# Performance work log

Hardware: AMD Instinct MI355X
Metric: run time of the kernel (lower is better)

The kernel has to match this reference:

```python
import jax, jax.numpy as jnp
import numpy as np

DIM = 512
NH = 16
HEAD = DIM // NH  # 32
WS1 = 8   # window_size // 2 (shift_h=True)
WS2 = 16  # window_size
SHIFT = 4  # window_size // 4


def _rotary(t, cos, sin):
    # t: (..., C); split even/odd channels, rotate, concat halves
    x1, x2 = t[..., 0::2], t[..., 1::2]
    return jnp.concatenate([x1 * cos - x2 * sin, x2 * cos + x1 * sin], axis=-1)


def setup_inputs() -> dict:
    key = jax.random.key(0)
    ks = jax.random.split(key, 8)
    B, H, W = 8, 64, 64
    G = (H // WS1) * (W // WS2)  # 32
    N = WS1 * WS2                # 128
    s = 1.0 / np.sqrt(DIM)
    return {
        "x": jax.random.normal(ks[0], (B, H, W, DIM), jnp.float32),
        "pos_embed_q": jax.random.normal(ks[1], (2, G, 1, N, HEAD // 2), jnp.float32),
        "pos_embed_kv": jax.random.normal(ks[2], (2, G, 1, 2 * N, HEAD // 2), jnp.float32),
        "mask": jnp.zeros((G, 1, N, 2 * N), jnp.float32),
        "w_q": jax.random.normal(ks[3], (DIM, DIM), jnp.float32) * s,
        "b_q": jnp.zeros((DIM,), jnp.float32),
        "w_kv": jax.random.normal(ks[4], (DIM, 2 * DIM), jnp.float32) * s,
        "b_kv": jnp.zeros((2 * DIM,), jnp.float32),
        "w_proj": jax.random.normal(ks[5], (DIM, DIM), jnp.float32) * s,
        "b_proj": jnp.zeros((DIM,), jnp.float32),
        "H": H,
        "W": W,
    }


def reference(x, pos_embed_q, pos_embed_kv, mask, w_q, b_q, w_kv, b_kv, w_proj, b_proj, H, W):
    B = x.shape[0]
    G = (H // WS1) * (W // WS2)
    N = WS1 * WS2
    C = HEAD

    # q projection + window partition -> (B, G, nH, N, C)
    q = x @ w_q + b_q
    q = q.reshape(B, H // WS1, WS1, W // WS2, WS2, NH, C)
    q = q.transpose(0, 1, 3, 5, 2, 4, 6).reshape(B, G, NH, N, C)

    # kv projection, two opposite rolls along H, window partition -> (2, B, G, nH, 2N, C)
    kv = x @ w_kv + b_kv                              # (B,H,W,2D)
    kvs = jnp.stack([jnp.roll(kv, -SHIFT, axis=1), jnp.roll(kv, SHIFT, axis=1)])  # (2shift,B,H,W,2D)
    kvs = kvs.reshape(2, B, H // WS1, WS1, W // WS2, WS2, 2, NH, C)
    kvs = kvs.transpose(6, 1, 2, 4, 7, 0, 3, 5, 8).reshape(2, B, G, NH, 2 * N, C)
    k, v = kvs[0], kvs[1]

    # rotary position embedding
    q = _rotary(q, pos_embed_q[0], pos_embed_q[1])
    k = _rotary(k, pos_embed_kv[0], pos_embed_kv[1])

    # scaled dot product attention with additive mask (eval: no dropout)
    scale = 1.0 / np.sqrt(C)
    scores = jnp.einsum('bgnqc,bgnkc->bgnqk', q, k) * scale + mask
    attn = jax.nn.softmax(scores, axis=-1)
    o = jnp.einsum('bgnqk,bgnkc->bgnqc', attn, v)     # (B,G,nH,N,C)

    # window un-partition -> (B, H, W, D), output projection
    o = o.reshape(B, H // WS1, W // WS2, NH, WS1, WS2, C)
    o = o.transpose(0, 1, 4, 2, 5, 3, 6).reshape(B, H, W, DIM)
    return o @ w_proj + b_proj
```

## Files before the change

### kernel.cpp

```cpp
#include <hip/hip_runtime.h>

typedef __bf16 bf16x8 __attribute__((ext_vector_type(8)));
typedef __bf16 bf16x4 __attribute__((ext_vector_type(4)));
typedef float f32x4 __attribute__((ext_vector_type(4)));

#define DEV __device__ __forceinline__

DEV f32x4 mfma16(bf16x8 a, bf16x8 b, f32x4 c) {
    return __builtin_amdgcn_mfma_f32_16x16x32_bf16(a, b, c, 0, 0, 0);
}

DEV void async16(const void* g, void* l) {
    __builtin_amdgcn_global_load_lds((__attribute__((address_space(1))) void*)g,
                                     (__attribute__((address_space(3))) void*)l, 16, 0, 0);
}

#define LDS_FENCE() asm volatile("" ::: "memory")

__global__ __launch_bounds__(256) void cast_x_kernel(const float4* __restrict__ in,
                                                     bf16x8* __restrict__ out) {
    int i = blockIdx.x * 256 + threadIdx.x;
    float4 a = in[2 * i], b = in[2 * i + 1];
    bf16x8 o;
    o[0] = (__bf16)a.x; o[1] = (__bf16)a.y; o[2] = (__bf16)a.z; o[3] = (__bf16)a.w;
    o[4] = (__bf16)b.x; o[5] = (__bf16)b.y; o[6] = (__bf16)b.z; o[7] = (__bf16)b.w;
    out[i] = o;
}

__global__ void transpose_cast_kernel(const float* __restrict__ src,
                                      __bf16* __restrict__ dst, int R, int C) {
    __shared__ float tile[32][33];
    int tx = threadIdx.x, ty = threadIdx.y;
    int c0 = blockIdx.x * 32, r0 = blockIdx.y * 32;
#pragma unroll
    for (int j = 0; j < 4; ++j)
        tile[ty + j * 8][tx] = src[(size_t)(r0 + ty + j * 8) * C + c0 + tx];
    __syncthreads();
#pragma unroll
    for (int j = 0; j < 4; ++j)
        dst[(size_t)(c0 + ty + j * 8) * R + r0 + tx] = (__bf16)tile[tx][ty + j * 8];
}

__global__ __launch_bounds__(256) void mask_flag_kernel(const float* __restrict__ mask,
                                                        int* __restrict__ flags) {
    int g = blockIdx.x;
    const float4* m4 = (const float4*)(mask + (size_t)g * 32768);
    int any = 0;
    for (int i = threadIdx.x; i < 8192; i += 256) {
        float4 v = m4[i];
        any |= (v.x != 0.f) | (v.y != 0.f) | (v.z != 0.f) | (v.w != 0.f);
    }
    any = __any(any) ? 1 : 0;
    __shared__ int s;
    if (threadIdx.x == 0) s = 0;
    __syncthreads();
    if ((threadIdx.x & 63) == 0 && any) atomicOr(&s, 1);
    __syncthreads();
    if (threadIdx.x == 0) flags[g] = s;
}

__global__ __launch_bounds__(256) void gemm_bt(const __bf16* __restrict__ A,
                                               const __bf16* __restrict__ Bt,
                                               const float* __restrict__ bias0,
                                               const float* __restrict__ bias1,
                                               void* __restrict__ Cout, int N, int mode) {
    __shared__ __bf16 As[128 * 64];
    __shared__ __bf16 Bs[128 * 64];
    const int tid = threadIdx.x;
    const int bm = blockIdx.x, bn = blockIdx.y;
    const int lane = tid & 63, wv = tid >> 6;
    const int quad = lane >> 4, l16 = lane & 15;
    const int wm = (wv & 1) * 64, wn = (wv >> 1) * 64;
    const __bf16* Abase = A + (size_t)bm * 128 * 512;
    const __bf16* Bbase = Bt + (size_t)bn * 128 * 512;
    f32x4 acc[4][4] = {};
    for (int kr = 0; kr < 8; ++kr) {
#pragma unroll
        for (int i = 0; i < 4; ++i) {
            int chunk = i * 256 + tid;
            int r = chunk >> 3, cc = chunk & 7;
            int src = cc ^ (r & 7);
            async16(Abase + r * 512 + kr * 64 + src * 8, &As[chunk * 8]);
            async16(Bbase + r * 512 + kr * 64 + src * 8, &Bs[chunk * 8]);
        }
        __syncthreads();
#pragma unroll
        for (int kk = 0; kk < 2; ++kk) {
            bf16x8 af[4], bfm[4];
#pragma unroll
            for (int t = 0; t < 4; ++t) {
                int ra = wm + t * 16 + l16, rb = wn + t * 16 + l16;
                int c = kk * 4 + quad;
                af[t]  = *(const bf16x8*)&As[ra * 64 + ((c ^ (ra & 7)) << 3)];
                bfm[t] = *(const bf16x8*)&Bs[rb * 64 + ((c ^ (rb & 7)) << 3)];
            }
#pragma unroll
            for (int mt = 0; mt < 4; ++mt)
#pragma unroll
                for (int nt = 0; nt < 4; ++nt)
                    acc[mt][nt] = mfma16(af[mt], bfm[nt], acc[mt][nt]);
        }
        __syncthreads();
    }
#pragma unroll
    for (int nt = 0; nt < 4; ++nt) {
        int ng = bn * 128 + wn + nt * 16 + l16;
        float bias = (ng < 512) ? bias0[ng] : bias1[ng - 512];
        if (mode == 0) {
            int type = ng >> 9, nhh = (ng >> 5) & 15, c = ng & 31;
            __bf16* dst = (__bf16*)Cout + (size_t)type * 16777216 + (size_t)nhh * 1048576 + c;
#pragma unroll
            for (int mt = 0; mt < 4; ++mt)
#pragma unroll
                for (int r = 0; r < 4; ++r) {
                    int mg = bm * 128 + wm + mt * 16 + quad * 4 + r;
                    dst[(size_t)mg * 32] = (__bf16)(acc[mt][nt][r] + bias);
                }
        } else {
#pragma unroll
            for (int mt = 0; mt < 4; ++mt)
#pragma unroll
                for (int r = 0; r < 4; ++r) {
                    int mg = bm * 128 + wm + mt * 16 + quad * 4 + r;
                    ((float*)Cout)[(size_t)mg * N + ng] = acc[mt][nt][r] + bias;
                }
        }
    }
}

#define ATT_SCALE 0.17677669529663687f

__global__ __launch_bounds__(256, 4) void attn_kernel(const __bf16* __restrict__ qkv,
                                                      const float* __restrict__ peq,
                                                      const float* __restrict__ pekv,
                                                      const float* __restrict__ mask,
                                                      const int* __restrict__ mflags,
                                                      __bf16* __restrict__ oatt) {
    __shared__ __align__(16) char smem[38400];
    __bf16* Ks = (__bf16*)smem;
    __bf16* Vt = (__bf16*)(smem + 16384);
    __bf16* Ps = (__bf16*)(smem + 33280);

    const int tid = threadIdx.x;
    const int bid = ((blockIdx.x & 7) << 9) | (blockIdx.x >> 3);
    const int b = bid >> 9;
    const int g = (bid >> 4) & 31;
    const int nh = bid & 15;
    const int gh = g >> 2, gw = g & 3;
    const int lane = tid & 63, wv = tid >> 6;
    const int quad = lane >> 4, l16 = lane & 15;

    const __bf16* qq = qkv + (size_t)nh * 1048576;
    const __bf16* kkp = qkv + 16777216 + (size_t)nh * 1048576;
    const __bf16* vvp = qkv + 33554432 + (size_t)nh * 1048576;

#pragma unroll
    for (int it = 0; it < 4; ++it) {
        int item = it * 256 + tid;
        int ko = item >> 2, c8 = item & 3;
        int roll = ko >> 7, n = ko & 127;
        int h = (gh * 8 + (n >> 4) + (roll ? 60 : 4)) & 63;
        int w = gw * 16 + (n & 15);
        int row = (b * 64 + h) * 64 + w;
        bf16x8 v = *(const bf16x8*)(kkp + (size_t)row * 32 + c8 * 8);
        int pidx = (g * 256 + ko) * 16 + c8 * 4;
        float4 c4 = *(const float4*)(pekv + pidx);
        float4 s4 = *(const float4*)(pekv + 131072 + pidx);
        float cs[4] = {c4.x, c4.y, c4.z, c4.w}, sn[4] = {s4.x, s4.y, s4.z, s4.w};
        bf16x4 lo, hi;
#pragma unroll
        for (int j = 0; j < 4; ++j) {
            float k0 = (float)v[2 * j], k1 = (float)v[2 * j + 1];
            lo[j] = (__bf16)(k0 * cs[j] - k1 * sn[j]);
            hi[j] = (__bf16)(k1 * cs[j] + k0 * sn[j]);
        }
        int sw = (ko >> 1) & 3;
        int base = ko * 32, off = (c8 & 1) * 4;
        *(bf16x4*)&Ks[base + (((c8 >> 1) ^ sw) << 3) + off]       = lo;
        *(bf16x4*)&Ks[base + (((2 + (c8 >> 1)) ^ sw) << 3) + off] = hi;
    }
#pragma unroll
    for (int it = 0; it < 4; ++it) {
        int ko = tid;
        int roll = ko >> 7, n = ko & 127;
        int h = (gh * 8 + (n >> 4) + (roll ? 60 : 4)) & 63;
        int w = gw * 16 + (n & 15);
        int row = (b * 64 + h) * 64 + w;
        bf16x8 v = *(const bf16x8*)(vvp + (size_t)row * 32 + it * 8);
#pragma unroll
        for (int j = 0; j < 8; ++j)
            Vt[(it * 8 + j) * 264 + ko] = v[j];
    }

    bf16x8 aq[2];
    {
        const int halfsel = quad & 1;
        const bool hi_half = quad >= 2;
#pragma unroll
        for (int rt = 0; rt < 2; ++rt) {
            int n = wv * 32 + rt * 16 + l16;
            int h = gh * 8 + (n >> 4), w = gw * 16 + (n & 15);
            int row = (b * 64 + h) * 64 + w;
            const __bf16* qp = qq + (size_t)row * 32 + halfsel * 16;
            bf16x8 rA = *(const bf16x8*)qp;
            bf16x8 rB = *(const bf16x8*)(qp + 8);
            int pb = (g * 128 + n) * 16 + halfsel * 8;
            float4 ca = *(const float4*)(peq + pb);
            float4 cb = *(const float4*)(peq + pb + 4);
            float4 sa = *(const float4*)(peq + 65536 + pb);
            float4 sb = *(const float4*)(peq + 65536 + pb + 4);
            float cc[8] = {ca.x, ca.y, ca.z, ca.w, cb.x, cb.y, cb.z, cb.w};
            float ss[8] = {sa.x, sa.y, sa.z, sa.w, sb.x, sb.y, sb.z, sb.w};
#pragma unroll
            for (int j = 0; j < 8; ++j) {
                float q0 = (float)(j < 4 ? rA[2 * j] : rB[2 * (j - 4)]);
                float q1 = (float)(j < 4 ? rA[2 * j + 1] : rB[2 * (j - 4) + 1]);
                float r = hi_half ? (q1 * cc[j] + q0 * ss[j]) : (q0 * cc[j] - q1 * ss[j]);
                aq[rt][j] = (__bf16)(r * ATT_SCALE);
            }
        }
    }
    __syncthreads();

    f32x4 o00 = {}, o01 = {}, o10 = {}, o11 = {};
    f32x4 rs0 = {}, rs1 = {};
    const bool use_mask = mflags[g] != 0;
    const float* mg = mask + (size_t)g * 32768;
    __bf16* Pw = Ps + wv * 640;
    const int arow = l16 * 40 + quad * 8;

#pragma unroll 2
    for (int ch = 0; ch < 8; ++ch) {
        bf16x8 vb0 = *(const bf16x8*)&Vt[l16 * 264 + ch * 32 + quad * 8];
        bf16x8 vb1 = *(const bf16x8*)&Vt[(16 + l16) * 264 + ch * 32 + quad * 8];
        f32x4 z = {0.f, 0.f, 0.f, 0.f};
        int key0 = ch * 32 + l16, key1 = key0 + 16;
        bf16x8 bk0 = *(const bf16x8*)&Ks[key0 * 32 + ((quad ^ ((key0 >> 1) & 3)) << 3)];
        bf16x8 bk1 = *(const bf16x8*)&Ks[key1 * 32 + ((quad ^ ((key1 >> 1) & 3)) << 3)];
        f32x4 s00 = mfma16(aq[0], bk0, z), s01 = mfma16(aq[0], bk1, z);
        f32x4 s10 = mfma16(aq[1], bk0, z), s11 = mfma16(aq[1], bk1, z);

        if (use_mask) {
#pragma unroll
            for (int r = 0; r < 4; ++r) {
                int r0 = (wv * 32 + quad * 4 + r) * 256 + ch * 32 + l16;
                int r1 = (wv * 32 + 16 + quad * 4 + r) * 256 + ch * 32 + l16;
                s00[r] += mg[r0];      s01[r] += mg[r0 + 16];
                s10[r] += mg[r1];      s11[r] += mg[r1 + 16];
            }
        }
#pragma unroll
        for (int r = 0; r < 4; ++r) {
            s00[r] = __expf(s00[r]); s01[r] = __expf(s01[r]);
            s10[r] = __expf(s10[r]); s11[r] = __expf(s11[r]);
            rs0[r] += s00[r] + s01[r];
            rs1[r] += s10[r] + s11[r];
        }
#pragma unroll
        for (int r = 0; r < 4; ++r) {
            Pw[(quad * 4 + r) * 40 + l16]      = (__bf16)s00[r];
            Pw[(quad * 4 + r) * 40 + 16 + l16] = (__bf16)s01[r];
        }
        LDS_FENCE();
        bf16x8 a0 = *(const bf16x8*)&Pw[arow];
        LDS_FENCE();
#pragma unroll
        for (int r = 0; r < 4; ++r) {
            Pw[(quad * 4 + r) * 40 + l16]      = (__bf16)s10[r];
            Pw[(quad * 4 + r) * 40 + 16 + l16] = (__bf16)s11[r];
        }
        LDS_FENCE();
        bf16x8 a1 = *(const bf16x8*)&Pw[arow];
        LDS_FENCE();
        o00 = mfma16(a0, vb0, o00); o01 = mfma16(a0, vb1, o01);
        o10 = mfma16(a1, vb0, o10); o11 = mfma16(a1, vb1, o11);
    }

#pragma unroll
    for (int off = 1; off < 16; off <<= 1) {
#pragma unroll
        for (int r = 0; r < 4; ++r) {
            rs0[r] += __shfl_xor(rs0[r], off);
            rs1[r] += __shfl_xor(rs1[r], off);
        }
    }
#pragma unroll
    for (int r = 0; r < 4; ++r) { rs0[r] = 1.f / rs0[r]; rs1[r] = 1.f / rs1[r]; }

#pragma unroll
    for (int r = 0; r < 4; ++r) {
        {
            int rown = wv * 32 + quad * 4 + r;
            int h = gh * 8 + (rown >> 4), w = gw * 16 + (rown & 15);
            size_t base = ((size_t)(b * 64 + h) * 64 + w) * 512 + nh * 32;
            oatt[base + l16]      = (__bf16)(o00[r] * rs0[r]);
            oatt[base + 16 + l16] = (__bf16)(o01[r] * rs0[r]);
        }
        {
            int rown = wv * 32 + 16 + quad * 4 + r;
            int h = gh * 8 + (rown >> 4), w = gw * 16 + (rown & 15);
            size_t base = ((size_t)(b * 64 + h) * 64 + w) * 512 + nh * 32;
            oatt[base + l16]      = (__bf16)(o10[r] * rs1[r]);
            oatt[base + 16 + l16] = (__bf16)(o11[r] * rs1[r]);
        }
    }
}

extern "C" void kernel_launch(void* const* d_in, const int* in_sizes, int n_in,
                              void* d_out, int out_size, void* d_ws, size_t ws_size,
                              hipStream_t stream) {
    const float* x     = (const float*)d_in[0];
    const float* peq   = (const float*)d_in[1];
    const float* pekv  = (const float*)d_in[2];
    const float* mask  = (const float*)d_in[3];
    const float* wq    = (const float*)d_in[4];
    const float* bq    = (const float*)d_in[5];
    const float* wkv   = (const float*)d_in[6];
    const float* bkv   = (const float*)d_in[7];
    const float* wproj = (const float*)d_in[8];
    const float* bproj = (const float*)d_in[9];
    float* out = (float*)d_out;

    char* ws = (char*)d_ws;
    __bf16* xb    = (__bf16*)(ws);
    __bf16* oatt  = (__bf16*)(ws);
    __bf16* wqkvT = (__bf16*)(ws + 33554432);
    int*    mflag = (int*)(ws + 33554432);
    __bf16* wpT   = (__bf16*)(ws + 35127296);
    __bf16* qkv   = (__bf16*)(ws + 35651584);

    cast_x_kernel<<<8192, 256, 0, stream>>>((const float4*)x, (bf16x8*)xb);
    transpose_cast_kernel<<<dim3(16, 16), dim3(32, 8), 0, stream>>>(wq, wqkvT, 512, 512);
    transpose_cast_kernel<<<dim3(32, 16), dim3(32, 8), 0, stream>>>(wkv, wqkvT + 512 * 512, 512, 1024);
    transpose_cast_kernel<<<dim3(16, 16), dim3(32, 8), 0, stream>>>(wproj, wpT, 512, 512);

    gemm_bt<<<dim3(256, 12), 256, 0, stream>>>(xb, wqkvT, bq, bkv, qkv, 1536, 0);
    mask_flag_kernel<<<32, 256, 0, stream>>>(mask, mflag);
    attn_kernel<<<4096, 256, 0, stream>>>(qkv, peq, pekv, mask, mflag, oatt);
    gemm_bt<<<dim3(256, 4), 256, 0, stream>>>(oatt, wpT, bproj, bproj, out, 512, 1);
}
```

Measured before the change: 327.0 us.

## Replace GEMM with 256x256 tiled, double-buffered LDS pipeline and 512 threads

```diff
diff --git a/kernel.cpp b/kernel.cpp
--- a/kernel.cpp
+++ b/kernel.cpp
@@ -16,6 +16,8 @@
 }
 
 #define LDS_FENCE() asm volatile("" ::: "memory")
+#define BARRIER() asm volatile("s_barrier" ::: "memory")
+#define VMCNT(n) asm volatile("s_waitcnt vmcnt(" #n ")" ::: "memory")
 
 __global__ __launch_bounds__(256) void cast_x_kernel(const float4* __restrict__ in,
                                                      bf16x8* __restrict__ out) {
@@ -59,69 +61,100 @@
     if (threadIdx.x == 0) flags[g] = s;
 }
 
-__global__ __launch_bounds__(256) void gemm_bt(const __bf16* __restrict__ A,
-                                               const __bf16* __restrict__ Bt,
-                                               const float* __restrict__ bias0,
-                                               const float* __restrict__ bias1,
-                                               void* __restrict__ Cout, int N, int mode) {
-    __shared__ __bf16 As[128 * 64];
-    __shared__ __bf16 Bs[128 * 64];
+__global__ __launch_bounds__(512, 2) void gemm256(const __bf16* __restrict__ A,
+                                                  const __bf16* __restrict__ Bt,
+                                                  const float* __restrict__ bias0,
+                                                  const float* __restrict__ bias1,
+                                                  void* __restrict__ Cout, int N, int mode) {
+    __shared__ __bf16 As[2][256 * 64];
+    __shared__ __bf16 Bs[2][256 * 64];
     const int tid = threadIdx.x;
     const int bm = blockIdx.x, bn = blockIdx.y;
     const int lane = tid & 63, wv = tid >> 6;
     const int quad = lane >> 4, l16 = lane & 15;
-    const int wm = (wv & 1) * 64, wn = (wv >> 1) * 64;
-    const __bf16* Abase = A + (size_t)bm * 128 * 512;
-    const __bf16* Bbase = Bt + (size_t)bn * 128 * 512;
-    f32x4 acc[4][4] = {};
-    for (int kr = 0; kr < 8; ++kr) {
-#pragma unroll
-        for (int i = 0; i < 4; ++i) {
-            int chunk = i * 256 + tid;
-            int r = chunk >> 3, cc = chunk & 7;
-            int src = cc ^ (r & 7);
-            async16(Abase + r * 512 + kr * 64 + src * 8, &As[chunk * 8]);
-            async16(Bbase + r * 512 + kr * 64 + src * 8, &Bs[chunk * 8]);
-        }
-        __syncthreads();
-#pragma unroll
-        for (int kk = 0; kk < 2; ++kk) {
-            bf16x8 af[4], bfm[4];
+    const int wm = (wv >> 2) * 128, wn = (wv & 3) * 64;
+    const __bf16* Abase = A + (size_t)bm * 256 * 512;
+    const __bf16* Bbase = Bt + (size_t)bn * 256 * 512;
+
+    int s_off[4];
+#pragma unroll
+    for (int i = 0; i < 4; ++i) {
+        int chunk = i * 512 + tid;
+        int r = chunk >> 3, cc = chunk & 7;
+        s_off[i] = r * 512 + ((cc ^ (r & 7)) << 3);
+    }
+
+    f32x4 acc[8][4] = {};
+
+#pragma unroll
+    for (int i = 0; i < 4; ++i) {
+        int chunk = i * 512 + tid;
+        async16(Abase + s_off[i], &As[0][chunk * 8]);
+        async16(Bbase + s_off[i], &Bs[0][chunk * 8]);
+    }
+
+    for (int kt = 0; kt < 8; ++kt) {
+        const int c = kt & 1;
+        if (kt < 7) {
+#pragma unroll
+            for (int i = 0; i < 4; ++i) {
+                int chunk = i * 512 + tid;
+                async16(Abase + s_off[i] + (kt + 1) * 64, &As[c ^ 1][chunk * 8]);
+                async16(Bbase + s_off[i] + (kt + 1) * 64, &Bs[c ^ 1][chunk * 8]);
+            }
+            VMCNT(8);
+        } else {
+            VMCNT(0);
+        }
+        BARRIER();
+
+        const __bf16* Ab = &As[c][0];
+        const __bf16* Bb = &Bs[c][0];
+#pragma unroll
+        for (int ks = 0; ks < 2; ++ks) {
+            bf16x8 af[8], bfm[4];
+            const int cch = ks * 4 + quad;
+#pragma unroll
+            for (int t = 0; t < 8; ++t) {
+                int ra = wm + t * 16 + l16;
+                af[t] = *(const bf16x8*)&Ab[ra * 64 + ((cch ^ (ra & 7)) << 3)];
+            }
 #pragma unroll
             for (int t = 0; t < 4; ++t) {
-                int ra = wm + t * 16 + l16, rb = wn + t * 16 + l16;
-                int c = kk * 4 + quad;
-                af[t]  = *(const bf16x8*)&As[ra * 64 + ((c ^ (ra & 7)) << 3)];
-                bfm[t] = *(const bf16x8*)&Bs[rb * 64 + ((c ^ (rb & 7)) << 3)];
-            }
-#pragma unroll
-            for (int mt = 0; mt < 4; ++mt)
+                int rb = wn + t * 16 + l16;
+                bfm[t] = *(const bf16x8*)&Bb[rb * 64 + ((cch ^ (rb & 7)) << 3)];
+            }
+            __builtin_amdgcn_s_setprio(1);
+#pragma unroll
+            for (int mt = 0; mt < 8; ++mt)
 #pragma unroll
                 for (int nt = 0; nt < 4; ++nt)
                     acc[mt][nt] = mfma16(af[mt], bfm[nt], acc[mt][nt]);
-        }
-        __syncthreads();
-    }
+            __builtin_amdgcn_s_setprio(0);
+            BARRIER();
+        }
+    }
+
 #pragma unroll
     for (int nt = 0; nt < 4; ++nt) {
-        int ng = bn * 128 + wn + nt * 16 + l16;
+        int ng = bn * 256 + wn + nt * 16 + l16;
         float bias = (ng < 512) ? bias0[ng] : bias1[ng - 512];
         if (mode == 0) {
-            int type = ng >> 9, nhh = (ng >> 5) & 15, c = ng & 31;
-            __bf16* dst = (__bf16*)Cout + (size_t)type * 16777216 + (size_t)nhh * 1048576 + c;
-#pragma unroll
-            for (int mt = 0; mt < 4; ++mt)
+            int type = ng >> 9, nhh = (ng >> 5) & 15, ch = ng & 31;
+            __bf16* dst = (__bf16*)Cout + (size_t)type * 16777216 + (size_t)nhh * 1048576 + ch;
+#pragma unroll
+            for (int mt = 0; mt < 8; ++mt)
 #pragma unroll
                 for (int r = 0; r < 4; ++r) {
-                    int mg = bm * 128 + wm + mt * 16 + quad * 4 + r;
+                    int mg = bm * 256 + wm + mt * 16 + quad * 4 + r;
                     dst[(size_t)mg * 32] = (__bf16)(acc[mt][nt][r] + bias);
                 }
         } else {
 #pragma unroll
-            for (int mt = 0; mt < 4; ++mt)
+            for (int mt = 0; mt < 8; ++mt)
 #pragma unroll
                 for (int r = 0; r < 4; ++r) {
-                    int mg = bm * 128 + wm + mt * 16 + quad * 4 + r;
+                    int mg = bm * 256 + wm + mt * 16 + quad * 4 + r;
                     ((float*)Cout)[(size_t)mg * N + ng] = acc[mt][nt][r] + bias;
                 }
         }
@@ -334,8 +367,8 @@
     transpose_cast_kernel<<<dim3(32, 16), dim3(32, 8), 0, stream>>>(wkv, wqkvT + 512 * 512, 512, 1024);
     transpose_cast_kernel<<<dim3(16, 16), dim3(32, 8), 0, stream>>>(wproj, wpT, 512, 512);
 
-    gemm_bt<<<dim3(256, 12), 256, 0, stream>>>(xb, wqkvT, bq, bkv, qkv, 1536, 0);
+    gemm256<<<dim3(128, 6), 512, 0, stream>>>(xb, wqkvT, bq, bkv, qkv, 1536, 0);
     mask_flag_kernel<<<32, 256, 0, stream>>>(mask, mflag);
     attn_kernel<<<4096, 256, 0, stream>>>(qkv, peq, pekv, mask, mflag, oatt);
-    gemm_bt<<<dim3(256, 4), 256, 0, stream>>>(oatt, wpT, bproj, bproj, out, 512, 1);
-}
+    gemm256<<<dim3(128, 2), 512, 0, stream>>>(oatt, wpT, bproj, bproj, out, 512, 1);
+}
```

Result: faster. 317.6 us (-2.9%).

## Double-buffer GEMM LDS tiles with async prefetch and XCD-aware block remapping

Applied to the files above, without the earlier changes.

```diff
diff --git a/kernel.cpp b/kernel.cpp
--- a/kernel.cpp
+++ b/kernel.cpp
@@ -16,6 +16,8 @@
 }
 
 #define LDS_FENCE() asm volatile("" ::: "memory")
+#define BARRIER() asm volatile("s_barrier" ::: "memory")
+#define VMCNT(n) asm volatile("s_waitcnt vmcnt(" #n ")" ::: "memory")
 
 __global__ __launch_bounds__(256) void cast_x_kernel(const float4* __restrict__ in,
                                                      bf16x8* __restrict__ out) {
@@ -59,56 +61,83 @@
     if (threadIdx.x == 0) flags[g] = s;
 }
 
-__global__ __launch_bounds__(256) void gemm_bt(const __bf16* __restrict__ A,
-                                               const __bf16* __restrict__ Bt,
-                                               const float* __restrict__ bias0,
-                                               const float* __restrict__ bias1,
-                                               void* __restrict__ Cout, int N, int mode) {
-    __shared__ __bf16 As[128 * 64];
-    __shared__ __bf16 Bs[128 * 64];
+__global__ __launch_bounds__(256, 2) void gemm128(const __bf16* __restrict__ A,
+                                                  const __bf16* __restrict__ Bt,
+                                                  const float* __restrict__ bias0,
+                                                  const float* __restrict__ bias1,
+                                                  void* __restrict__ Cout, int N, int mode) {
+    __shared__ __bf16 As[2][128 * 64];
+    __shared__ __bf16 Bs[2][128 * 64];
     const int tid = threadIdx.x;
-    const int bm = blockIdx.x, bn = blockIdx.y;
+    const int nbn = N >> 7;
+    const int per_xcd = gridDim.x >> 3;
+    const int w = (blockIdx.x & 7) * per_xcd + (blockIdx.x >> 3);
+    const int bm = w / nbn, bn = w % nbn;
     const int lane = tid & 63, wv = tid >> 6;
     const int quad = lane >> 4, l16 = lane & 15;
     const int wm = (wv & 1) * 64, wn = (wv >> 1) * 64;
     const __bf16* Abase = A + (size_t)bm * 128 * 512;
     const __bf16* Bbase = Bt + (size_t)bn * 128 * 512;
     f32x4 acc[4][4] = {};
+
+    int s_off[4];
+#pragma unroll
+    for (int i = 0; i < 4; ++i) {
+        int chunk = i * 256 + tid;
+        int r = chunk >> 3, cc = chunk & 7;
+        s_off[i] = r * 512 + ((cc ^ (r & 7)) << 3);
+    }
+
+#pragma unroll
+    for (int i = 0; i < 4; ++i) {
+        int chunk = i * 256 + tid;
+        async16(Abase + s_off[i], &As[0][chunk * 8]);
+        async16(Bbase + s_off[i], &Bs[0][chunk * 8]);
+    }
+
+#pragma unroll
     for (int kr = 0; kr < 8; ++kr) {
-#pragma unroll
-        for (int i = 0; i < 4; ++i) {
-            int chunk = i * 256 + tid;
-            int r = chunk >> 3, cc = chunk & 7;
-            int src = cc ^ (r & 7);
-            async16(Abase + r * 512 + kr * 64 + src * 8, &As[chunk * 8]);
-            async16(Bbase + r * 512 + kr * 64 + src * 8, &Bs[chunk * 8]);
-        }
-        __syncthreads();
+        const int c = kr & 1;
+        if (kr < 7) {
+#pragma unroll
+            for (int i = 0; i < 4; ++i) {
+                int chunk = i * 256 + tid;
+                async16(Abase + s_off[i] + (kr + 1) * 64, &As[c ^ 1][chunk * 8]);
+                async16(Bbase + s_off[i] + (kr + 1) * 64, &Bs[c ^ 1][chunk * 8]);
+            }
+            VMCNT(8);
+        } else {
+            VMCNT(0);
+        }
+        BARRIER();
 #pragma unroll
         for (int kk = 0; kk < 2; ++kk) {
             bf16x8 af[4], bfm[4];
 #pragma unroll
             for (int t = 0; t < 4; ++t) {
                 int ra = wm + t * 16 + l16, rb = wn + t * 16 + l16;
-                int c = kk * 4 + quad;
-                af[t]  = *(const bf16x8*)&As[ra * 64 + ((c ^ (ra & 7)) << 3)];
-                bfm[t] = *(const bf16x8*)&Bs[rb * 64 + ((c ^ (rb & 7)) << 3)];
+                int cch = kk * 4 + quad;
+                af[t]  = *(const bf16x8*)&As[c][ra * 64 + ((cch ^ (ra & 7)) << 3)];
+                bfm[t] = *(const bf16x8*)&Bs[c][rb * 64 + ((cch ^ (rb & 7)) << 3)];
             }
+            __builtin_amdgcn_s_setprio(1);
 #pragma unroll
             for (int mt = 0; mt < 4; ++mt)
 #pragma unroll
                 for (int nt = 0; nt < 4; ++nt)
                     acc[mt][nt] = mfma16(af[mt], bfm[nt], acc[mt][nt]);
-        }
-        __syncthreads();
-    }
+            __builtin_amdgcn_s_setprio(0);
+        }
+        BARRIER();
+    }
+
 #pragma unroll
     for (int nt = 0; nt < 4; ++nt) {
         int ng = bn * 128 + wn + nt * 16 + l16;
         float bias = (ng < 512) ? bias0[ng] : bias1[ng - 512];
         if (mode == 0) {
-            int type = ng >> 9, nhh = (ng >> 5) & 15, c = ng & 31;
-            __bf16* dst = (__bf16*)Cout + (size_t)type * 16777216 + (size_t)nhh * 1048576 + c;
+            int type = ng >> 9, nhh = (ng >> 5) & 15, ch = ng & 31;
+            __bf16* dst = (__bf16*)Cout + (size_t)type * 16777216 + (size_t)nhh * 1048576 + ch;
 #pragma unroll
             for (int mt = 0; mt < 4; ++mt)
 #pragma unroll
@@ -334,8 +363,8 @@
     transpose_cast_kernel<<<dim3(32, 16), dim3(32, 8), 0, stream>>>(wkv, wqkvT + 512 * 512, 512, 1024);
     transpose_cast_kernel<<<dim3(16, 16), dim3(32, 8), 0, stream>>>(wproj, wpT, 512, 512);
 
-    gemm_bt<<<dim3(256, 12), 256, 0, stream>>>(xb, wqkvT, bq, bkv, qkv, 1536, 0);
+    gemm128<<<3072, 256, 0, stream>>>(xb, wqkvT, bq, bkv, qkv, 1536, 0);
     mask_flag_kernel<<<32, 256, 0, stream>>>(mask, mflag);
     attn_kernel<<<4096, 256, 0, stream>>>(qkv, peq, pekv, mask, mflag, oatt);
-    gemm_bt<<<dim3(256, 4), 256, 0, stream>>>(oatt, wpT, bproj, bproj, out, 512, 1);
-}
+    gemm128<<<1024, 256, 0, stream>>>(oatt, wpT, bproj, bproj, out, 512, 1);
+}
```

Measured after the change: 295.6 us. 1.11x faster.
